# Kernel optimization log

Hardware: AMD Instinct MI355X
Metric: run time of the kernel (lower is better)

Reference implementation:

```python
import jax, jax.numpy as jnp
import numpy as np

N_MESH = 40962  # icosahedral level-6 mesh nodes (x[..., -40962:])


def _lin_coords(out_size, in_size, scale):
    # torch F.interpolate bilinear, align_corners=False source coords
    i = jnp.arange(out_size, dtype=jnp.float32)
    src = jnp.maximum((i + 0.5) / scale - 0.5, 0.0)
    i0 = jnp.clip(jnp.floor(src).astype(jnp.int32), 0, in_size - 1)
    i1 = jnp.minimum(i0 + 1, in_size - 1)
    w = src - i0.astype(jnp.float32)
    return i0, i1, w


def _bilinear4(x):
    # x: (B,C,H,W) -> (B,C,4H,4W), separable bilinear, align_corners=False
    B, C, H, W = x.shape
    i0, i1, wh = _lin_coords(4 * H, H, 4.0)
    x = x[:, :, i0, :] * (1.0 - wh)[None, None, :, None] + x[:, :, i1, :] * wh[None, None, :, None]
    j0, j1, ww = _lin_coords(4 * W, W, 4.0)
    x = x[:, :, :, j0] * (1.0 - ww) + x[:, :, :, j1] * ww
    return x


def _grid2mesh(x, lat, lon):
    # x: (B,C,H,W); drop last lat row, upsample x4, append broadcast pole row
    B, C, H, W = x.shape
    pole = x[:, :, -1, 0][:, :, None, None] * jnp.ones((B, C, 1, 4 * W), x.dtype)
    xi = _bilinear4(x[:, :, :-1, :])            # (B,C,4(H-1),4W)
    xi = jnp.concatenate([xi, pole], axis=2)    # (B,C,4(H-1)+1,4W)
    return xi[:, :, lat - 1, lon - 1]           # (B,C,M) gather at mesh coords


def _gcn(h, W, b, src, dst, norm, n):
    # GCNConv: sym-normalized scatter-add aggregation of linearly transformed feats
    h = h @ W                                    # (B,N,Hd)
    msg = lambda hb: jax.ops.segment_sum(hb[src] * norm[:, None], dst, num_segments=n)
    return jax.vmap(msg)(h) + b


def reference(x, edge_index, Lat, Lon, W1, b1, W2, b2, Wl, bl, Wl1, bl1):
    B, C, H, Wd = x.shape
    mesh = _grid2mesh(x, Lat, Lon)                               # (B,C,M)
    feats = jnp.concatenate([x.reshape(B, C, H * Wd), mesh], -1)  # (B,C,N)
    h = feats.transpose(0, 2, 1)                                 # (B,N,C)
    n = h.shape[1]

    # gcn_norm with self loops (edge_weight = 1)
    loops = jnp.arange(n, dtype=edge_index.dtype)
    src = jnp.concatenate([edge_index[0], loops])
    dst = jnp.concatenate([edge_index[1], loops])
    deg = jax.ops.segment_sum(jnp.ones(src.shape, h.dtype), dst, num_segments=n)
    dinv = jnp.where(deg > 0, deg ** -0.5, 0.0)
    norm = dinv[src] * dinv[dst]

    h = _gcn(h, W1, b1, src, dst, norm, n)
    h = jax.nn.gelu(h, approximate=False)
    h = _gcn(h, W2, b2, src, dst, norm, n)
    h = h[:, -N_MESH:, :]                                        # keep mesh nodes
    out = jax.nn.gelu((h @ Wl + bl) @ Wl1 + bl1, approximate=False)
    return out.transpose(0, 2, 1)                                # (B,out_ch,M)


def setup_inputs() -> dict:
    key = jax.random.key(0)
    ks = jax.random.split(key, 16)
    B, C, H, W = 1, 69, 181, 360
    HID, OUT = 256, 256
    N = H * W + N_MESH  # 106122
    E = 500000
    x = jax.random.normal(ks[0], (B, C, H, W), jnp.float32)
    edge_index = jax.random.randint(ks[1], (2, E), 0, N, dtype=jnp.int64)
    Lat = jax.random.randint(ks[2], (N_MESH,), 1, 4 * (H - 1) + 2, dtype=jnp.int64)
    Lon = jax.random.randint(ks[3], (N_MESH,), 1, 4 * W + 1, dtype=jnp.int64)
    s = 0.05
    return {
        "x": x, "edge_index": edge_index, "Lat": Lat, "Lon": Lon,
        "W1": jax.random.normal(ks[4], (C, HID), jnp.float32) * s,
        "b1": jnp.zeros((HID,), jnp.float32),
        "W2": jax.random.normal(ks[5], (HID, HID), jnp.float32) * s,
        "b2": jnp.zeros((HID,), jnp.float32),
        "Wl": jax.random.normal(ks[6], (HID, 256), jnp.float32) * s,
        "bl": jnp.zeros((256,), jnp.float32),
        "Wl1": jax.random.normal(ks[7], (256, OUT), jnp.float32) * s,
        "bl1": jnp.zeros((OUT,), jnp.float32),
    }
```

## Files before the change

### kernel.cpp

```cpp
#include <hip/hip_runtime.h>

#define NGRID 65160
#define NMESH 40962
#define NTOT  (NGRID + NMESH)
#define CIN   69
#define KPAD1 96
#define HID   256
#define HH    181
#define WWID  360
#define SCAN_BS 1024
#define NBLK_SCAN ((NTOT + SCAN_BS - 1) / SCAN_BS)

#define NT1TILES ((NTOT + 63) / 64)
#define NT1PAD   (NT1TILES * 64)
#define NT2TILES ((NMESH + 63) / 64)
#define NT2PAD   (NT2TILES * 64)

#define TXBLKS  ((NGRID + 63) / 64)
#define DEGBLKS ((NTOT + 255) / 256)
#define MAXD    12

#define W1OFF  0
#define WCOFF  (96 * 256)
#define WALLK  (96 + 256)

typedef float f32x4 __attribute__((ext_vector_type(4)));
typedef _Float16 f16;
typedef _Float16 f16x2 __attribute__((ext_vector_type(2)));
typedef _Float16 f16x4 __attribute__((ext_vector_type(4)));
typedef _Float16 f16x8 __attribute__((ext_vector_type(8)));

__device__ __forceinline__ float gelu_exact(float v) {
    return 0.5f * v * (1.0f + erff(v * 0.7071067811865476f));
}
__device__ __forceinline__ float gelu_fast(float v) {
    float u = v * fmaf(v * v, 0.07135481283f, 1.5957691216f);
    return v * __builtin_amdgcn_rcpf(1.0f + __expf(-u));
}

__global__ __launch_bounds__(256) void transpose_x(const float* __restrict__ x,
                                                   f16* __restrict__ h0g,
                                                   float* __restrict__ deg,
                                                   int* __restrict__ cnt) {
    if (blockIdx.x >= TXBLKS) {
        int i = (blockIdx.x - TXBLKS) * 256 + threadIdx.x;
        if (i < NTOT) { deg[i] = 1.0f; cnt[i] = 0; }
        return;
    }
    __shared__ float tile[96][65];
    int s0 = blockIdx.x * 64;
    int t = threadIdx.x;
#pragma unroll
    for (int i = 0; i < 24; ++i) {
        int idx = t + i * 256;
        int c = idx >> 6, s = idx & 63;
        int gs = s0 + s;
        float v = 0.f;
        if (c < CIN && gs < NGRID) v = x[(size_t)c * NGRID + gs];
        tile[c][s] = v;
    }
    __syncthreads();
#pragma unroll
    for (int i = 0; i < 12; ++i) {
        int idx = t + i * 256;
        int r = idx / 48, u = idx % 48;
        int gr = s0 + r;
        if (gr < NGRID) {
            f16x2 p;
            p.x = (f16)tile[u * 2 + 0][r];
            p.y = (f16)tile[u * 2 + 1][r];
            ((f16x2*)h0g)[(size_t)gr * 48 + u] = p;
        }
    }
}

__global__ __launch_bounds__(256) void mesh_interp(const f16* __restrict__ h0g,
                                                   const int* __restrict__ Lat,
                                                   const int* __restrict__ Lon,
                                                   f16* __restrict__ h0m) {
    int t = blockIdx.x * 256 + threadIdx.x;
    if (t >= NMESH * 48) return;
    int j = t / 48, u = t % 48;
    int la = Lat[j] - 1;
    int lo = Lon[j] - 1;
    const f16x2* g = (const f16x2*)h0g;
    f16x2 o;
    if (la == 720) {
        o = g[(size_t)(180 * WWID) * 48 + u];
    } else {
        float sh = fmaxf((la + 0.5f) * 0.25f - 0.5f, 0.0f);
        int i0 = min((int)sh, HH - 2);
        int i1 = min(i0 + 1, HH - 2);
        float wh = sh - (float)i0;
        float sw = fmaxf((lo + 0.5f) * 0.25f - 0.5f, 0.0f);
        int j0 = min((int)sw, WWID - 1);
        int j1 = min(j0 + 1, WWID - 1);
        float ww = sw - (float)j0;
        f16x2 v00 = g[(size_t)(i0 * WWID + j0) * 48 + u];
        f16x2 v10 = g[(size_t)(i1 * WWID + j0) * 48 + u];
        f16x2 v01 = g[(size_t)(i0 * WWID + j1) * 48 + u];
        f16x2 v11 = g[(size_t)(i1 * WWID + j1) * 48 + u];
        float ax = (float)v00.x + ((float)v10.x - (float)v00.x) * wh;
        float ay = (float)v00.y + ((float)v10.y - (float)v00.y) * wh;
        float bx = (float)v01.x + ((float)v11.x - (float)v01.x) * wh;
        float by = (float)v01.y + ((float)v11.y - (float)v01.y) * wh;
        o.x = (f16)(ax + (bx - ax) * ww);
        o.y = (f16)(ay + (by - ay) * ww);
    }
    ((f16x2*)h0m)[(size_t)j * 48 + u] = o;
}

__global__ void deg_scatter(const int* __restrict__ ei, float* __restrict__ deg, int E) {
    int e = blockIdx.x * 256 + threadIdx.x;
    if (e < E) atomicAdd(&deg[ei[E + e]], 1.0f);
}

__global__ __launch_bounds__(SCAN_BS) void scan1(const float* __restrict__ deg,
                                                 float* __restrict__ dinv,
                                                 int* __restrict__ off, int* __restrict__ bsum) {
    __shared__ int s[SCAN_BS];
    int t = threadIdx.x;
    int i = blockIdx.x * SCAN_BS + t;
    int v = (i < NTOT) ? ((int)deg[i] - 1) : 0;
    if (i < NTOT) dinv[i] = 1.0f / sqrtf((float)(v + 1));
    s[t] = v; __syncthreads();
    for (int d = 1; d < SCAN_BS; d <<= 1) {
        int x = (t >= d) ? s[t - d] : 0;
        __syncthreads();
        s[t] += x;
        __syncthreads();
    }
    if (i < NTOT) off[i] = s[t] - v;
    if (t == SCAN_BS - 1) bsum[blockIdx.x] = s[t];
}
__global__ void scan2(int* __restrict__ bsum) {
    __shared__ int s[128];
    int t = threadIdx.x;
    int v = (t < NBLK_SCAN) ? bsum[t] : 0;
    s[t] = v; __syncthreads();
    for (int d = 1; d < 128; d <<= 1) {
        int x = (t >= d) ? s[t - d] : 0;
        __syncthreads();
        s[t] += x;
        __syncthreads();
    }
    if (t < NBLK_SCAN) bsum[t] = s[t] - v;
}
__global__ __launch_bounds__(SCAN_BS) void scan3(int* __restrict__ off, const int* __restrict__ bsum) {
    int i = blockIdx.x * SCAN_BS + threadIdx.x;
    if (i < NTOT) off[i] += bsum[blockIdx.x];
}

__global__ void csr_fill(const int* __restrict__ ei, const float* __restrict__ dinv,
                         const int* __restrict__ off, int* __restrict__ cnt,
                         int2* __restrict__ epk, int E) {
    int e = blockIdx.x * 256 + threadIdx.x;
    if (e >= E) return;
    int s = ei[e], d = ei[E + e];
    int pos = off[d] + atomicAdd(&cnt[d], 1);
    epk[pos] = make_int2(s, __float_as_int(dinv[s] * dinv[d]));
}

__global__ __launch_bounds__(256) void wgemm(const float* __restrict__ A,
                                             const float* __restrict__ B,
                                             float* __restrict__ C) {
    __shared__ float As[16][68];
    __shared__ float Bs[16][64];
    int r0 = blockIdx.y * 64, c0 = blockIdx.x * 64;
    int t = threadIdx.x;
    int tr = t >> 4, tc = t & 15;
    float acc[4][4] = {};
    for (int kk = 0; kk < 256; kk += 16) {
#pragma unroll
        for (int i = 0; i < 4; ++i) {
            int idx = t + i * 256;
            int r = idx >> 4, k = idx & 15;
            As[k][r] = A[(size_t)(r0 + r) * 256 + kk + k];
        }
#pragma unroll
        for (int i = 0; i < 4; ++i) {
            int idx = t + i * 256;
            int k = idx >> 6, c = idx & 63;
            Bs[k][c] = B[(size_t)(kk + k) * 256 + c0 + c];
        }
        __syncthreads();
#pragma unroll
        for (int k = 0; k < 16; ++k) {
            float a[4], b[4];
#pragma unroll
            for (int i = 0; i < 4; ++i) a[i] = As[k][tr * 4 + i];
#pragma unroll
            for (int j = 0; j < 4; ++j) b[j] = Bs[k][tc * 4 + j];
#pragma unroll
            for (int i = 0; i < 4; ++i)
#pragma unroll
                for (int j = 0; j < 4; ++j) acc[i][j] = fmaf(a[i], b[j], acc[i][j]);
        }
        __syncthreads();
    }
#pragma unroll
    for (int i = 0; i < 4; ++i)
#pragma unroll
        for (int j = 0; j < 4; ++j)
            C[(size_t)(r0 + tr * 4 + i) * 256 + c0 + tc * 4 + j] = acc[i][j];
}

__global__ __launch_bounds__(256) void bias_k(const float* __restrict__ b2,
                                              const float* __restrict__ M1,
                                              const float* __restrict__ bl,
                                              const float* __restrict__ Wl1,
                                              const float* __restrict__ bl1,
                                              float* __restrict__ bc) {
    int c = threadIdx.x;
    float acc = bl1[c];
    for (int j = 0; j < 256; ++j) {
        acc = fmaf(b2[j], M1[(size_t)j * 256 + c], acc);
        acc = fmaf(bl[j], Wl1[(size_t)j * 256 + c], acc);
    }
    bc[c] = acc;
}

__global__ void pack_f16(const float* __restrict__ W1, const float* __restrict__ Wc,
                         f16* __restrict__ wp) {
    int t = blockIdx.x * 256 + threadIdx.x;
    if (t >= WALLK * HID) return;
    int kg = t >> 8, c = t & 255;
    float v;
    size_t idx;
    if (kg < 96) {
        v = (kg < CIN) ? W1[(size_t)kg * HID + c] : 0.f;
        idx = W1OFF + ((((size_t)(kg >> 3)) * HID + c) << 3) + (kg & 7);
    } else {
        int ks = kg - 96;
        int kl = ((ks & 15) << 4) | (ks >> 4);
        v = Wc[(size_t)kl * HID + c];
        idx = WCOFF + ((((size_t)(ks >> 3)) * HID + c) << 3) + (ks & 7);
    }
    wp[idx] = (f16)v;
}

__global__ __launch_bounds__(256) void agg1(const f16* __restrict__ h0,
                                            const float* __restrict__ deg,
                                            const float* __restrict__ dinv,
                                            const int* __restrict__ off,
                                            const int2* __restrict__ epk,
                                            f16* __restrict__ P0) {
    int wv = (blockIdx.x * 256 + threadIdx.x) >> 6;
    if (wv >= NT1PAD) return;
    int lane = threadIdx.x & 63;
    if (lane >= 48) return;
    int r = wv & 63, tile = wv >> 6;
    char* dst = (char*)P0 + (size_t)tile * 12288 + ((r * 192 + lane * 4) ^ ((r & 7) << 4));
    if (wv >= NTOT) { *(unsigned*)dst = 0u; return; }
    int d = wv;
    const f16x2* g = (const f16x2*)h0;
    float dv = dinv[d];
    float w2 = dv * dv;
    f16x2 v = g[(size_t)d * 48 + lane];
    float ax = w2 * (float)v.x;
    float ay = w2 * (float)v.y;
    const int2* ep = epk + off[d];
    int n = (int)deg[d] - 1;
    int2 e[MAXD];
    f16x2 u[MAXD];
#pragma unroll
    for (int p = 0; p < MAXD; ++p) if (p < n) e[p] = ep[p];
#pragma unroll
    for (int p = 0; p < MAXD; ++p) if (p < n) u[p] = g[(size_t)e[p].x * 48 + lane];
#pragma unroll
    for (int p = 0; p < MAXD; ++p) if (p < n) {
        float w = __int_as_float(e[p].y);
        ax = fmaf(w, (float)u[p].x, ax);
        ay = fmaf(w, (float)u[p].y, ay);
    }
    for (int p = MAXD; p < n; ++p) {
        int2 ee = ep[p];
        f16x2 uu = g[(size_t)ee.x * 48 + lane];
        float w = __int_as_float(ee.y);
        ax = fmaf(w, (float)uu.x, ax);
        ay = fmaf(w, (float)uu.y, ay);
    }
    f16x2 o; o.x = (f16)ax; o.y = (f16)ay;
    *(f16x2*)dst = o;
}

__global__ __launch_bounds__(256) void agg2(const f16* __restrict__ A,
                                            const float* __restrict__ deg,
                                            const float* __restrict__ dinv,
                                            const int* __restrict__ off,
                                            const int2* __restrict__ epk,
                                            f16* __restrict__ P2) {
    int wv = (blockIdx.x * 256 + threadIdx.x) >> 6;
    if (wv >= NT2PAD) return;
    int lane = threadIdx.x & 63;
    int r = wv & 63, tile = wv >> 6;
    char* dst = (char*)P2 + (size_t)tile * 32768 + ((r * 512 + lane * 8) ^ ((r & 7) << 4));
    if (wv >= NMESH) { *(unsigned long long*)dst = 0ull; return; }
    int d = NGRID + wv;
    const f16x4* g = (const f16x4*)A;
    float dv = dinv[d];
    float w2 = dv * dv;
    f16x4 v = g[(size_t)d * 64 + lane];
    float4 acc;
    acc.x = w2 * (float)v.x; acc.y = w2 * (float)v.y;
    acc.z = w2 * (float)v.z; acc.w = w2 * (float)v.w;
    const int2* ep = epk + off[d];
    int n = (int)deg[d] - 1;
    int2 e[MAXD];
    f16x4 u[MAXD];
#pragma unroll
    for (int p = 0; p < MAXD; ++p) if (p < n) e[p] = ep[p];
#pragma unroll
    for (int p = 0; p < MAXD; ++p) if (p < n) u[p] = g[(size_t)e[p].x * 64 + lane];
#pragma unroll
    for (int p = 0; p < MAXD; ++p) if (p < n) {
        float w = __int_as_float(e[p].y);
        acc.x = fmaf(w, (float)u[p].x, acc.x); acc.y = fmaf(w, (float)u[p].y, acc.y);
        acc.z = fmaf(w, (float)u[p].z, acc.z); acc.w = fmaf(w, (float)u[p].w, acc.w);
    }
    for (int p = MAXD; p < n; ++p) {
        int2 ee = ep[p];
        f16x4 uu = g[(size_t)ee.x * 64 + lane];
        float w = __int_as_float(ee.y);
        acc.x = fmaf(w, (float)uu.x, acc.x); acc.y = fmaf(w, (float)uu.y, acc.y);
        acc.z = fmaf(w, (float)uu.z, acc.z); acc.w = fmaf(w, (float)uu.w, acc.w);
    }
    f16x4 o;
    o.x = (f16)acc.x; o.y = (f16)acc.y; o.z = (f16)acc.z; o.w = (f16)acc.w;
    *(f16x4*)dst = o;
}

__global__ __launch_bounds__(256) void gemm1_f16(const f16* __restrict__ P0,
                                                 const f16* __restrict__ wp,
                                                 const float* __restrict__ bias,
                                                 f16* __restrict__ Af) {
    const int wid = (blockIdx.x * 256 + threadIdx.x) >> 6;
    const int lane = threadIdx.x & 63;
    const int l15 = lane & 15, l4 = lane >> 4;
    const int tile = wid >> 3;
    const int rb = (wid >> 1) & 3;
    const int ch = wid & 1;
    if (tile >= NT1TILES) return;

    f16x8 a[3];
    {
        const char* base = (const char*)P0 + (size_t)tile * 12288;
        int r = rb * 16 + l15;
#pragma unroll
        for (int ks = 0; ks < 3; ++ks) {
            int byte = r * 192 + (ks * 32 + l4 * 8) * 2;
            a[ks] = *(const f16x8*)(base + (byte ^ ((r & 7) << 4)));
        }
    }

    f32x4 acc[8];
#pragma unroll
    for (int j = 0; j < 8; ++j) acc[j] = (f32x4)0.f;
#pragma unroll
    for (int j = 0; j < 8; ++j) {
        int c = (ch * 8 + j) * 16 + l15;
#pragma unroll
        for (int ks = 0; ks < 3; ++ks) {
            size_t o = ((((size_t)ks << 2) + l4) * HID + c) << 3;
            f16x8 w = *(const f16x8*)(wp + W1OFF + o);
            acc[j] = __builtin_amdgcn_mfma_f32_16x16x32_f16(a[ks], w, acc[j], 0, 0, 0);
        }
    }

    float bv[8];
#pragma unroll
    for (int j = 0; j < 8; ++j) bv[j] = bias[(ch * 8 + j) * 16 + l15];

    const int gr0 = tile * 64 + rb * 16 + l4 * 4;
#pragma unroll
    for (int reg = 0; reg < 4; ++reg) {
        int gr = gr0 + reg;
        if (gr < NTOT) {
            f16x8 o;
#pragma unroll
            for (int j = 0; j < 8; ++j)
                o[j] = (f16)gelu_fast(acc[j][reg] + bv[j]);
            *(f16x8*)(Af + (size_t)gr * HID + l15 * 16 + ch * 8) = o;
        }
    }
}

__global__ __launch_bounds__(256) void final_k(const f16* __restrict__ P2,
                                               const f16* __restrict__ wp,
                                               const float* __restrict__ bc,
                                               float* __restrict__ out) {
    __shared__ __align__(16) f16 Ps[64 * 256];
    const int tile = blockIdx.x;
    const int row0 = tile * 64;
    const int t = threadIdx.x;
    const int lane = t & 63;
    const int wave = t >> 6;
    const int l15 = lane & 15, l4 = lane >> 4;
    const int cw = wave * 64;
    const char* src = (const char*)P2 + (size_t)tile * 32768;
#pragma unroll
    for (int i = 0; i < 8; ++i) {
        int o = t * 16 + i * 4096;
        *(uint4*)((char*)Ps + o) = *(const uint4*)(src + o);
    }
    __syncthreads();
    f32x4 acc[4][4] = {};
#pragma unroll
    for (int ks = 0; ks < 256; ks += 32) {
        f16x8 w[4], p[4];
#pragma unroll
        for (int mb = 0; mb < 4; ++mb) {
            int c = cw + mb * 16 + l15;
            size_t off = ((((size_t)ks >> 3) + l4) * HID + c) << 3;
            w[mb] = *(const f16x8*)(wp + WCOFF + off);
        }
#pragma unroll
        for (int jb = 0; jb < 4; ++jb) {
            int r = jb * 16 + l15;
            int byte = r * 512 + (ks + l4 * 8) * 2;
            int swz = byte ^ ((r & 7) << 4);
            p[jb] = *(f16x8*)((char*)Ps + swz);
        }
#pragma unroll
        for (int mb = 0; mb < 4; ++mb)
#pragma unroll
            for (int jb = 0; jb < 4; ++jb)
                acc[mb][jb] = __builtin_amdgcn_mfma_f32_16x16x32_f16(w[mb], p[jb], acc[mb][jb], 0, 0, 0);
    }
    const bool full = (row0 + 64 <= NMESH);
#pragma unroll
    for (int mb = 0; mb < 4; ++mb) {
#pragma unroll
        for (int r = 0; r < 4; ++r) {
            int c = cw + mb * 16 + l4 * 4 + r;
            float bv = bc[c];
            float* orow = out + (size_t)c * NMESH + row0;
#pragma unroll
            for (int jb = 0; jb < 4; ++jb) {
                int j = jb * 16 + l15;
                float v = gelu_fast(acc[mb][jb][r] + bv);
                if (full || row0 + j < NMESH) orow[j] = v;
            }
        }
    }
}

extern "C" void kernel_launch(void* const* d_in, const int* in_sizes, int n_in,
                              void* d_out, int out_size, void* d_ws, size_t ws_size,
                              hipStream_t stream) {
    const float* x   = (const float*)d_in[0];
    const int*   ei  = (const int*)d_in[1];
    const int*   Lat = (const int*)d_in[2];
    const int*   Lon = (const int*)d_in[3];
    const float* W1  = (const float*)d_in[4];
    const float* b1  = (const float*)d_in[5];
    const float* W2  = (const float*)d_in[6];
    const float* b2  = (const float*)d_in[7];
    const float* Wl  = (const float*)d_in[8];
    const float* bl  = (const float*)d_in[9];
    const float* Wl1 = (const float*)d_in[10];
    const float* bl1 = (const float*)d_in[11];
    float* out = (float*)d_out;
    const int E = in_sizes[1] / 2;

    f16*   h0  = (f16*)d_out;
    int2*  epk = (int2*)((char*)d_out + (size_t)NTOT * KPAD1 * 2);

    f16*   P0   = (f16*)d_ws;
    f16*   Af   = P0 + (size_t)NT1TILES * 6144;
    f16*   P2   = Af + (size_t)NTOT * HID;
    float* deg  = (float*)(P2 + (size_t)NT2TILES * 16384);
    float* dinv = deg + NTOT;
    int*   off  = (int*)(dinv + NTOT);
    int*   cnt  = off + NTOT;
    int*   bsum = cnt + NTOT;
    float* M1   = (float*)(bsum + 128);
    float* WcF  = M1 + HID * HID;
    float* bc   = WcF + HID * HID;
    f16*   wp   = (f16*)(bc + HID);

    transpose_x<<<TXBLKS + DEGBLKS, 256, 0, stream>>>(x, h0, deg, cnt);
    mesh_interp<<<(NMESH * 48 + 255) / 256, 256, 0, stream>>>(h0, Lat, Lon,
                                                              h0 + (size_t)NGRID * KPAD1);

    deg_scatter<<<(E + 255) / 256, 256, 0, stream>>>(ei, deg, E);
    scan1<<<NBLK_SCAN, SCAN_BS, 0, stream>>>(deg, dinv, off, bsum);
    scan2<<<1, 128, 0, stream>>>(bsum);
    scan3<<<NBLK_SCAN, SCAN_BS, 0, stream>>>(off, bsum);
    csr_fill<<<(E + 255) / 256, 256, 0, stream>>>(ei, dinv, off, cnt, epk, E);

    dim3 gW(4, 4);
    wgemm<<<gW, 256, 0, stream>>>(Wl, Wl1, M1);
    wgemm<<<gW, 256, 0, stream>>>(W2, M1, WcF);
    bias_k<<<1, 256, 0, stream>>>(b2, M1, bl, Wl1, bl1, bc);
    pack_f16<<<(WALLK * HID + 255) / 256, 256, 0, stream>>>(W1, WcF, wp);

    agg1<<<(int)(((long long)NT1PAD * 64 + 255) / 256), 256, 0, stream>>>(
        h0, deg, dinv, off, epk, P0);
    gemm1_f16<<<(NT1TILES * 8 * 64 + 255) / 256, 256, 0, stream>>>(P0, wp, b1, Af);

    agg2<<<(int)(((long long)NT2PAD * 64 + 255) / 256), 256, 0, stream>>>(
        Af, deg, dinv, off, epk, P2);

    final_k<<<NT2TILES, 256, 0, stream>>>(P2, wp, bc, out);
}
```

Baseline: 273.2 us.

## Factor GCN normalization into row scaling and store source-only CSR edges

```diff
diff --git a/kernel.cpp b/kernel.cpp
--- a/kernel.cpp
+++ b/kernel.cpp
@@ -18,7 +18,6 @@
 
 #define TXBLKS  ((NGRID + 63) / 64)
 #define DEGBLKS ((NTOT + 255) / 256)
-#define MAXD    12
 
 #define W1OFF  0
 #define WCOFF  (96 * 256)
@@ -30,9 +29,6 @@
 typedef _Float16 f16x4 __attribute__((ext_vector_type(4)));
 typedef _Float16 f16x8 __attribute__((ext_vector_type(8)));
 
-__device__ __forceinline__ float gelu_exact(float v) {
-    return 0.5f * v * (1.0f + erff(v * 0.7071067811865476f));
-}
 __device__ __forceinline__ float gelu_fast(float v) {
     float u = v * fmaf(v * v, 0.07135481283f, 1.5957691216f);
     return v * __builtin_amdgcn_rcpf(1.0f + __expf(-u));
@@ -133,32 +129,44 @@
     if (i < NTOT) off[i] = s[t] - v;
     if (t == SCAN_BS - 1) bsum[blockIdx.x] = s[t];
 }
-__global__ void scan2(int* __restrict__ bsum) {
+__global__ __launch_bounds__(SCAN_BS) void scan3(int* __restrict__ off, const int* __restrict__ bsum) {
     __shared__ int s[128];
     int t = threadIdx.x;
-    int v = (t < NBLK_SCAN) ? bsum[t] : 0;
-    s[t] = v; __syncthreads();
+    if (t < 128) s[t] = (t < NBLK_SCAN) ? bsum[t] : 0;
+    __syncthreads();
     for (int d = 1; d < 128; d <<= 1) {
-        int x = (t >= d) ? s[t - d] : 0;
+        int x = 0;
+        if (t < 128 && t >= d) x = s[t - d];
         __syncthreads();
-        s[t] += x;
+        if (t < 128) s[t] += x;
         __syncthreads();
     }
-    if (t < NBLK_SCAN) bsum[t] = s[t] - v;
-}
-__global__ __launch_bounds__(SCAN_BS) void scan3(int* __restrict__ off, const int* __restrict__ bsum) {
-    int i = blockIdx.x * SCAN_BS + threadIdx.x;
-    if (i < NTOT) off[i] += bsum[blockIdx.x];
-}
-
-__global__ void csr_fill(const int* __restrict__ ei, const float* __restrict__ dinv,
-                         const int* __restrict__ off, int* __restrict__ cnt,
-                         int2* __restrict__ epk, int E) {
+    int base = (blockIdx.x == 0) ? 0 : s[blockIdx.x - 1];
+    int i = blockIdx.x * SCAN_BS + t;
+    if (i < NTOT) off[i] += base;
+}
+
+__global__ __launch_bounds__(256) void scale_h0(f16* __restrict__ h0,
+                                                const float* __restrict__ dinv) {
+    long long t = (long long)blockIdx.x * 256 + threadIdx.x;
+    if (t >= (long long)NTOT * 24) return;
+    int row = (int)(t / 24);
+    float s = dinv[row];
+    f16x4 v = ((f16x4*)h0)[t];
+    v.x = (f16)((float)v.x * s);
+    v.y = (f16)((float)v.y * s);
+    v.z = (f16)((float)v.z * s);
+    v.w = (f16)((float)v.w * s);
+    ((f16x4*)h0)[t] = v;
+}
+
+__global__ void csr_fill(const int* __restrict__ ei, const int* __restrict__ off,
+                         int* __restrict__ cnt, int* __restrict__ esrc, int E) {
     int e = blockIdx.x * 256 + threadIdx.x;
     if (e >= E) return;
     int s = ei[e], d = ei[E + e];
     int pos = off[d] + atomicAdd(&cnt[d], 1);
-    epk[pos] = make_int2(s, __float_as_int(dinv[s] * dinv[d]));
+    esrc[pos] = s;
 }
 
 __global__ __launch_bounds__(256) void wgemm(const float* __restrict__ A,
@@ -243,7 +251,7 @@
                                             const float* __restrict__ deg,
                                             const float* __restrict__ dinv,
                                             const int* __restrict__ off,
-                                            const int2* __restrict__ epk,
+                                            const int* __restrict__ esrc,
                                             f16* __restrict__ P0) {
     int wv = (blockIdx.x * 256 + threadIdx.x) >> 6;
     if (wv >= NT1PAD) return;
@@ -254,33 +262,28 @@
     if (wv >= NTOT) { *(unsigned*)dst = 0u; return; }
     int d = wv;
     const f16x2* g = (const f16x2*)h0;
+    f16x2 v = g[(size_t)d * 48 + lane];
+    float ax = (float)v.x;
+    float ay = (float)v.y;
+    const int* ep = esrc + off[d];
+    int n = (int)deg[d] - 1;
+    int p = 0;
+    for (; p + 4 <= n; p += 4) {
+        int e0 = ep[p], e1 = ep[p + 1], e2 = ep[p + 2], e3 = ep[p + 3];
+        f16x2 u0 = g[(size_t)e0 * 48 + lane];
+        f16x2 u1 = g[(size_t)e1 * 48 + lane];
+        f16x2 u2 = g[(size_t)e2 * 48 + lane];
+        f16x2 u3 = g[(size_t)e3 * 48 + lane];
+        ax += (float)u0.x + (float)u1.x + (float)u2.x + (float)u3.x;
+        ay += (float)u0.y + (float)u1.y + (float)u2.y + (float)u3.y;
+    }
+    for (; p < n; ++p) {
+        f16x2 u = g[(size_t)ep[p] * 48 + lane];
+        ax += (float)u.x;
+        ay += (float)u.y;
+    }
     float dv = dinv[d];
-    float w2 = dv * dv;
-    f16x2 v = g[(size_t)d * 48 + lane];
-    float ax = w2 * (float)v.x;
-    float ay = w2 * (float)v.y;
-    const int2* ep = epk + off[d];
-    int n = (int)deg[d] - 1;
-    int2 e[MAXD];
-    f16x2 u[MAXD];
-#pragma unroll
-    for (int p = 0; p < MAXD; ++p) if (p < n) e[p] = ep[p];
-#pragma unroll
-    for (int p = 0; p < MAXD; ++p) if (p < n) u[p] = g[(size_t)e[p].x * 48 + lane];
-#pragma unroll
-    for (int p = 0; p < MAXD; ++p) if (p < n) {
-        float w = __int_as_float(e[p].y);
-        ax = fmaf(w, (float)u[p].x, ax);
-        ay = fmaf(w, (float)u[p].y, ay);
-    }
-    for (int p = MAXD; p < n; ++p) {
-        int2 ee = ep[p];
-        f16x2 uu = g[(size_t)ee.x * 48 + lane];
-        float w = __int_as_float(ee.y);
-        ax = fmaf(w, (float)uu.x, ax);
-        ay = fmaf(w, (float)uu.y, ay);
-    }
-    f16x2 o; o.x = (f16)ax; o.y = (f16)ay;
+    f16x2 o; o.x = (f16)(dv * ax); o.y = (f16)(dv * ay);
     *(f16x2*)dst = o;
 }
 
@@ -288,7 +291,7 @@
                                             const float* __restrict__ deg,
                                             const float* __restrict__ dinv,
                                             const int* __restrict__ off,
-                                            const int2* __restrict__ epk,
+                                            const int* __restrict__ esrc,
                                             f16* __restrict__ P2) {
     int wv = (blockIdx.x * 256 + threadIdx.x) >> 6;
     if (wv >= NT2PAD) return;
@@ -298,41 +301,40 @@
     if (wv >= NMESH) { *(unsigned long long*)dst = 0ull; return; }
     int d = NGRID + wv;
     const f16x4* g = (const f16x4*)A;
-    float dv = dinv[d];
-    float w2 = dv * dv;
     f16x4 v = g[(size_t)d * 64 + lane];
     float4 acc;
-    acc.x = w2 * (float)v.x; acc.y = w2 * (float)v.y;
-    acc.z = w2 * (float)v.z; acc.w = w2 * (float)v.w;
-    const int2* ep = epk + off[d];
+    acc.x = (float)v.x; acc.y = (float)v.y;
+    acc.z = (float)v.z; acc.w = (float)v.w;
+    const int* ep = esrc + off[d];
     int n = (int)deg[d] - 1;
-    int2 e[MAXD];
-    f16x4 u[MAXD];
-#pragma unroll
-    for (int p = 0; p < MAXD; ++p) if (p < n) e[p] = ep[p];
-#pragma unroll
-    for (int p = 0; p < MAXD; ++p) if (p < n) u[p] = g[(size_t)e[p].x * 64 + lane];
-#pragma unroll
-    for (int p = 0; p < MAXD; ++p) if (p < n) {
-        float w = __int_as_float(e[p].y);
-        acc.x = fmaf(w, (float)u[p].x, acc.x); acc.y = fmaf(w, (float)u[p].y, acc.y);
-        acc.z = fmaf(w, (float)u[p].z, acc.z); acc.w = fmaf(w, (float)u[p].w, acc.w);
-    }
-    for (int p = MAXD; p < n; ++p) {
-        int2 ee = ep[p];
-        f16x4 uu = g[(size_t)ee.x * 64 + lane];
-        float w = __int_as_float(ee.y);
-        acc.x = fmaf(w, (float)uu.x, acc.x); acc.y = fmaf(w, (float)uu.y, acc.y);
-        acc.z = fmaf(w, (float)uu.z, acc.z); acc.w = fmaf(w, (float)uu.w, acc.w);
-    }
+    int p = 0;
+    for (; p + 4 <= n; p += 4) {
+        int e0 = ep[p], e1 = ep[p + 1], e2 = ep[p + 2], e3 = ep[p + 3];
+        f16x4 u0 = g[(size_t)e0 * 64 + lane];
+        f16x4 u1 = g[(size_t)e1 * 64 + lane];
+        f16x4 u2 = g[(size_t)e2 * 64 + lane];
+        f16x4 u3 = g[(size_t)e3 * 64 + lane];
+        acc.x += (float)u0.x + (float)u1.x + (float)u2.x + (float)u3.x;
+        acc.y += (float)u0.y + (float)u1.y + (float)u2.y + (float)u3.y;
+        acc.z += (float)u0.z + (float)u1.z + (float)u2.z + (float)u3.z;
+        acc.w += (float)u0.w + (float)u1.w + (float)u2.w + (float)u3.w;
+    }
+    for (; p < n; ++p) {
+        f16x4 u = g[(size_t)ep[p] * 64 + lane];
+        acc.x += (float)u.x; acc.y += (float)u.y;
+        acc.z += (float)u.z; acc.w += (float)u.w;
+    }
+    float dv = dinv[d];
     f16x4 o;
-    o.x = (f16)acc.x; o.y = (f16)acc.y; o.z = (f16)acc.z; o.w = (f16)acc.w;
+    o.x = (f16)(dv * acc.x); o.y = (f16)(dv * acc.y);
+    o.z = (f16)(dv * acc.z); o.w = (f16)(dv * acc.w);
     *(f16x4*)dst = o;
 }
 
 __global__ __launch_bounds__(256) void gemm1_f16(const f16* __restrict__ P0,
                                                  const f16* __restrict__ wp,
                                                  const float* __restrict__ bias,
+                                                 const float* __restrict__ dinv,
                                                  f16* __restrict__ Af) {
     const int wid = (blockIdx.x * 256 + threadIdx.x) >> 6;
     const int lane = threadIdx.x & 63;
@@ -372,14 +374,16 @@
     for (int j = 0; j < 8; ++j) bv[j] = bias[(ch * 8 + j) * 16 + l15];
 
     const int gr0 = tile * 64 + rb * 16 + l4 * 4;
+    float4 dvv = *(const float4*)(dinv + gr0);
 #pragma unroll
     for (int reg = 0; reg < 4; ++reg) {
         int gr = gr0 + reg;
         if (gr < NTOT) {
+            float dv = (reg == 0) ? dvv.x : (reg == 1) ? dvv.y : (reg == 2) ? dvv.z : dvv.w;
             f16x8 o;
 #pragma unroll
             for (int j = 0; j < 8; ++j)
-                o[j] = (f16)gelu_fast(acc[j][reg] + bv[j]);
+                o[j] = (f16)(gelu_fast(acc[j][reg] + bv[j]) * dv);
             *(f16x8*)(Af + (size_t)gr * HID + l15 * 16 + ch * 8) = o;
         }
     }
@@ -463,8 +467,8 @@
     float* out = (float*)d_out;
     const int E = in_sizes[1] / 2;
 
-    f16*   h0  = (f16*)d_out;
-    int2*  epk = (int2*)((char*)d_out + (size_t)NTOT * KPAD1 * 2);
+    f16*  h0   = (f16*)d_out;
+    int*  esrc = (int*)((char*)d_out + (size_t)NTOT * KPAD1 * 2);
 
     f16*   P0   = (f16*)d_ws;
     f16*   Af   = P0 + (size_t)NT1TILES * 6144;
@@ -485,9 +489,9 @@
 
     deg_scatter<<<(E + 255) / 256, 256, 0, stream>>>(ei, deg, E);
     scan1<<<NBLK_SCAN, SCAN_BS, 0, stream>>>(deg, dinv, off, bsum);
-    scan2<<<1, 128, 0, stream>>>(bsum);
     scan3<<<NBLK_SCAN, SCAN_BS, 0, stream>>>(off, bsum);
-    csr_fill<<<(E + 255) / 256, 256, 0, stream>>>(ei, dinv, off, cnt, epk, E);
+    scale_h0<<<(int)(((long long)NTOT * 24 + 255) / 256), 256, 0, stream>>>(h0, dinv);
+    csr_fill<<<(E + 255) / 256, 256, 0, stream>>>(ei, off, cnt, esrc, E);
 
     dim3 gW(4, 4);
     wgemm<<<gW, 256, 0, stream>>>(Wl, Wl1, M1);
@@ -496,11 +500,11 @@
     pack_f16<<<(WALLK * HID + 255) / 256, 256, 0, stream>>>(W1, WcF, wp);
 
     agg1<<<(int)(((long long)NT1PAD * 64 + 255) / 256), 256, 0, stream>>>(
-        h0, deg, dinv, off, epk, P0);
-    gemm1_f16<<<(NT1TILES * 8 * 64 + 255) / 256, 256, 0, stream>>>(P0, wp, b1, Af);
+        h0, deg, dinv, off, esrc, P0);
+    gemm1_f16<<<(NT1TILES * 8 * 64 + 255) / 256, 256, 0, stream>>>(P0, wp, b1, dinv, Af);
 
     agg2<<<(int)(((long long)NT2PAD * 64 + 255) / 256), 256, 0, stream>>>(
-        Af, deg, dinv, off, epk, P2);
+        Af, deg, dinv, off, esrc, P2);
 
     final_k<<<NT2TILES, 256, 0, stream>>>(P2, wp, bc, out);
 }
```

After: 251.4 us. -8.0%, faster.
